# Kernel optimization log

Hardware: AMD Instinct MI355X
Metric: run time of the kernel (lower is better)

## Reference

```python
import jax, jax.numpy as jnp
import numpy as np

NUM_Q_HEADS = 32
NUM_KV_HEADS = 8
GROUP = NUM_Q_HEADS // NUM_KV_HEADS  # 4, matches hardcoded repeat_interleave(repeats=4)
HEAD_DIM = 128
ROPE_BASE = 10000.0


def _rope_cos_sin(seq_len, head_dim, dtype):
    # [S, D/2] angle tables for rotate-half RoPE
    inv_freq = 1.0 / (ROPE_BASE ** (jnp.arange(0, head_dim, 2, dtype=jnp.float32) / head_dim))
    ang = jnp.arange(seq_len, dtype=jnp.float32)[:, None] * inv_freq[None, :]
    return jnp.cos(ang).astype(dtype), jnp.sin(ang).astype(dtype)


def _apply_rope(x, cos, sin):
    # x: [B, S, H, D]; cos/sin: [S, D/2] broadcast over batch & heads
    x1, x2 = jnp.split(x, 2, axis=-1)
    c = cos[None, :, None, :]
    s = sin[None, :, None, :]
    return jnp.concatenate([x1 * c - x2 * s, x2 * c + x1 * s], axis=-1)


def setup_inputs() -> dict:
    key = jax.random.key(0)
    k1, k2, k3 = jax.random.split(key, 3)
    B, S, E = 2, 2048, 4096
    x = jax.random.normal(k1, (B, S, E), dtype=jnp.float32)
    w_in = jax.random.normal(k2, (6144, E), dtype=jnp.float32) * 0.02   # torch Linear weight [out, in]
    w_out = jax.random.normal(k3, (E, E), dtype=jnp.float32) * 0.02
    return {"x": x, "w_in": w_in, "w_out": w_out}


def reference(x, w_in, w_out):
    B, S, E = x.shape
    D = HEAD_DIM
    qkv = jnp.einsum('bse,fe->bsf', x, w_in)  # [B, S, 6144]
    parts = jnp.split(qkv, GROUP + 2, axis=-1)  # 6 equal chunks of width E//GROUP
    q = jnp.concatenate(parts[:GROUP], axis=-1).reshape(B, S, NUM_Q_HEADS, D)
    k = parts[GROUP].reshape(B, S, NUM_KV_HEADS, D)
    v = parts[GROUP + 1].reshape(B, S, NUM_KV_HEADS, D)

    cos, sin = _rope_cos_sin(S, D, x.dtype)
    q = _apply_rope(q, cos, sin)
    k = _apply_rope(k, cos, sin)

    # GQA without materializing repeated K/V: group q heads by kv head.
    # repeat_interleave(k, 4, dim=2) maps q head h -> kv head h // 4, i.e. q view [B,S,HKV,G,D]
    qg = q.reshape(B, S, NUM_KV_HEADS, GROUP, D)
    scale = 1.0 / jnp.sqrt(jnp.asarray(D, dtype=x.dtype))
    scores = jnp.einsum('bqhgd,bkhd->bhgqk', qg, k) * scale  # [B, HKV, G, S, S]
    causal = jnp.tril(jnp.ones((S, S), dtype=bool))
    scores = jnp.where(causal[None, None, None, :, :], scores, jnp.asarray(-1e30, dtype=scores.dtype))
    probs = jax.nn.softmax(scores, axis=-1)
    out = jnp.einsum('bhgqk,bkhd->bqhgd', probs, v)  # [B, S, HKV, G, D]
    out = out.reshape(B, S, E)
    return jnp.einsum('bse,fe->bsf', out, w_out)
```

## Files before the change

### kernel.cpp

```cpp
#include <hip/hip_runtime.h>
#include <hip/hip_bf16.h>
#include <stdint.h>

typedef unsigned short u16;
typedef __bf16 bf16x8 __attribute__((ext_vector_type(8)));
typedef u16 u16x8 __attribute__((ext_vector_type(8)));
typedef float f32x4 __attribute__((ext_vector_type(4)));
typedef float f32x16 __attribute__((ext_vector_type(16)));
typedef uint32_t u32x4 __attribute__((ext_vector_type(4)));

#define DEV __device__ __forceinline__
#define SBAR() asm volatile("s_barrier" ::: "memory")

DEV u16 f2bf(float f) {
  uint32_t u = __builtin_bit_cast(uint32_t, f);
  return (u16)((u + 0x7FFFu + ((u >> 16) & 1u)) >> 16);
}
DEV float bf2f(u16 h) { return __builtin_bit_cast(float, (uint32_t)h << 16); }

DEV void gload_lds16(const void* g, void* l) {
  __builtin_amdgcn_global_load_lds((const __attribute__((address_space(1))) uint32_t*)g,
                                   (__attribute__((address_space(3))) uint32_t*)l, 16, 0, 0);
}

DEV uint32_t cvtpk(float lo, float hi) {
  uint32_t r;
  asm("v_cvt_pk_bf16_f32 %0, %1, %2" : "=v"(r) : "v"(lo), "v"(hi));
  return r;
}
DEV void plswap(uint32_t& a, uint32_t& b) {
  asm("v_permlane32_swap_b32 %0, %1" : "+v"(a), "+v"(b));
}

__global__ void cvt_bf16(const float* __restrict__ in, u16* __restrict__ out, int n) {
  int i = (blockIdx.x * 256 + threadIdx.x) * 8;
  if (i >= n) return;
  const float4* p = reinterpret_cast<const float4*>(in + i);
  float4 a = p[0], b = p[1];
  u16x8 o;
  o[0] = f2bf(a.x); o[1] = f2bf(a.y); o[2] = f2bf(a.z); o[3] = f2bf(a.w);
  o[4] = f2bf(b.x); o[5] = f2bf(b.y); o[6] = f2bf(b.z); o[7] = f2bf(b.w);
  *reinterpret_cast<u16x8*>(out + i) = o;
}

__global__ void rope_table(float* __restrict__ ct, float* __restrict__ st) {
  int i = blockIdx.x * 256 + threadIdx.x;
  int s = i >> 6, d = i & 63;
  float invf = powf(10000.0f, -(float)d * (1.0f / 64.0f));
  float ang = (float)s * invf;
  ct[i] = cosf(ang);
  st[i] = sinf(ang);
}

__global__ void rope_apply(u16* __restrict__ qkv, const float* __restrict__ ct, const float* __restrict__ st) {
  int idx = blockIdx.x * 256 + threadIdx.x;
  int grp = idx & 7;
  int head = (idx >> 3) % 40;
  int row = idx / 320;
  int s = row & 2047;
  size_t f0 = head < 32 ? (size_t)head * 128 : (size_t)4096 + (size_t)(head - 32) * 128;
  u16* p = qkv + (size_t)row * 6144 + f0 + grp * 8;
  u16x8 a = *reinterpret_cast<const u16x8*>(p);
  u16x8 b = *reinterpret_cast<const u16x8*>(p + 64);
  const float4* cp = reinterpret_cast<const float4*>(ct + s * 64 + grp * 8);
  const float4* sp = reinterpret_cast<const float4*>(st + s * 64 + grp * 8);
  float4 c0 = cp[0], c1 = cp[1], s0 = sp[0], s1 = sp[1];
  float cc[8] = {c0.x, c0.y, c0.z, c0.w, c1.x, c1.y, c1.z, c1.w};
  float ss[8] = {s0.x, s0.y, s0.z, s0.w, s1.x, s1.y, s1.z, s1.w};
  u16x8 o1, o2;
#pragma unroll
  for (int i = 0; i < 8; i++) {
    float x1 = bf2f(a[i]), x2 = bf2f(b[i]);
    o1[i] = f2bf(x1 * cc[i] - x2 * ss[i]);
    o2[i] = f2bf(x2 * cc[i] + x1 * ss[i]);
  }
  *reinterpret_cast<u16x8*>(p) = o1;
  *reinterpret_cast<u16x8*>(p + 64) = o2;
}

__global__ void prep_vt(const u16* __restrict__ qkv, u16* __restrict__ vtg) {
  int id = blockIdx.x;
  int j = id & 31, kvh = (id >> 5) & 7, b = id >> 8;
  const int tid = threadIdx.x;
  const size_t rowB = (size_t)b * 2048;
  u16* img = vtg + (size_t)id * 8192;
#pragma unroll
  for (int p = 0; p < 4; p++) {
    int lin = p * 256 + tid;
    int d = lin >> 3, c = lin & 7;
    const u16* src = qkv + (rowB + j * 64 + c * 8) * 6144 + 5120 + kvh * 128 + d;
    u16x8 v;
#pragma unroll
    for (int i = 0; i < 8; i++) v[i] = src[(size_t)i * 6144];
    *reinterpret_cast<u16x8*>(img + d * 64 + ((c ^ (d & 7)) << 3)) = v;
  }
}

DEV void store_c(float* C, size_t idx, float v) { C[idx] = v; }
DEV void store_c(u16* C, size_t idx, float v) { C[idx] = f2bf(v); }

template <typename OutT>
__global__ __launch_bounds__(512, 2) void gemm256(const u16* __restrict__ A, const u16* __restrict__ B,
                                                  OutT* __restrict__ C, int M, int N, int K, int ldc) {
  __shared__ __align__(16) u16 lds[65536];
  char* LB = (char*)lds;
  const int tid = threadIdx.x;
  const int w = tid >> 6, lane = tid & 63;
  const int l15 = lane & 15, l4 = lane >> 4;
  const int wm = w >> 2, wn = w & 3;

  int nwg = gridDim.x;
  int q = nwg >> 3, rr = nwg & 7;
  int xcd = blockIdx.x & 7, idx = blockIdx.x >> 3;
  int sw = (xcd < rr ? xcd * (q + 1) : rr * (q + 1) + (xcd - rr) * q) + idx;
  int gxn = N >> 8;
  int by = sw / gxn, bx = sw - by * gxn;
  const int row0 = by << 8, col0 = bx << 8;
  const int NT = K >> 6;

  const int srow = w * 8 + (lane >> 3);
  const int sc16 = (lane & 7) ^ ((lane >> 3) & 7);
  const u16* gA = A + (size_t)(row0 + srow) * K + sc16 * 8;
  const u16* gB = B + (size_t)(col0 + srow) * K + sc16 * 8;

  const int fl = (l15 & 7) << 4;
  const int aoff = (wm * 128 + l15) * 128 + l4 * 16;
  const int boff = (wn * 64 + l15) * 128 + l4 * 16;

  f32x4 acc[8][4] = {};
  bf16x8 fA[4][2], fB0[2][2], fBc[2][2];

#define STAGE_A(kt, h, base)                                                      \
  {                                                                               \
    const u16* g_ = gA + (size_t)((h)*128) * K + (size_t)(kt)*64;                 \
    gload_lds16(g_, (base) + (h)*16384 + w * 1024);                               \
    gload_lds16(g_ + (size_t)64 * K, (base) + (h)*16384 + 8192 + w * 1024);       \
  }
#define STAGE_B(kt, h, base)                                                      \
  {                                                                               \
    const u16* g_ = gB + (size_t)((h)*128) * K + (size_t)(kt)*64;                 \
    gload_lds16(g_, (base) + (h)*16384 + w * 1024);                               \
    gload_lds16(g_ + (size_t)64 * K, (base) + (h)*16384 + 8192 + w * 1024);       \
  }
#define MFMA_Q(FB, MH, NH)                                                        \
  _Pragma("unroll") for (int kk = 0; kk < 2; kk++) {                              \
    _Pragma("unroll") for (int mf = 0; mf < 4; mf++) {                            \
      _Pragma("unroll") for (int nf = 0; nf < 2; nf++) {                          \
        acc[(MH)*4 + mf][(NH)*2 + nf] = __builtin_amdgcn_mfma_f32_16x16x32_bf16(  \
            fA[mf][kk], FB[nf][kk], acc[(MH)*4 + mf][(NH)*2 + nf], 0, 0, 0);      \
      }                                                                           \
    }                                                                             \
  }

  STAGE_A(0, 0, LB);
  STAGE_A(0, 1, LB);
  STAGE_B(0, 0, LB + 65536);
  STAGE_B(0, 1, LB + 65536);
  STAGE_A(1, 0, LB + 32768);
  STAGE_B(1, 0, LB + 98304);
  STAGE_B(1, 1, LB + 98304);
  asm volatile("s_waitcnt vmcnt(6)" ::: "memory");
  SBAR();

  for (int t = 0; t < NT; ++t) {
    char* ac = LB + (t & 1) * 32768;
    char* bc = LB + 65536 + (t & 1) * 32768;
    char* an = LB + ((t + 1) & 1) * 32768;

#pragma unroll
    for (int mf = 0; mf < 4; mf++)
#pragma unroll
      for (int kk = 0; kk < 2; kk++)
        fA[mf][kk] = *(const bf16x8*)(ac + ((aoff + mf * 2048 + kk * 64) ^ fl));
#pragma unroll
    for (int nf = 0; nf < 2; nf++)
#pragma unroll
      for (int kk = 0; kk < 2; kk++)
        fB0[nf][kk] = *(const bf16x8*)(bc + ((boff + nf * 2048 + kk * 64) ^ fl));
    if (t + 1 < NT) STAGE_A(t + 1, 1, an);
    asm volatile("s_waitcnt lgkmcnt(8)" ::: "memory");
    SBAR();
    asm volatile("s_waitcnt lgkmcnt(0)" ::: "memory");
    __builtin_amdgcn_sched_barrier(0);
    __builtin_amdgcn_s_setprio(1);
    MFMA_Q(fB0, 0, 0);
    __builtin_amdgcn_s_setprio(0);
    SBAR();

#pragma unroll
    for (int nf = 0; nf < 2; nf++)
#pragma unroll
      for (int kk = 0; kk < 2; kk++)
        fBc[nf][kk] = *(const bf16x8*)(bc + ((boff + (nf + 2) * 2048 + kk * 64) ^ fl));
    SBAR();
    asm volatile("s_waitcnt lgkmcnt(0)" ::: "memory");
    __builtin_amdgcn_sched_barrier(0);
    __builtin_amdgcn_s_setprio(1);
    MFMA_Q(fBc, 0, 1);
    __builtin_amdgcn_s_setprio(0);
    SBAR();

#pragma unroll
    for (int mf = 0; mf < 4; mf++)
#pragma unroll
      for (int kk = 0; kk < 2; kk++)
        fA[mf][kk] = *(const bf16x8*)(ac + ((aoff + (mf + 4) * 2048 + kk * 64) ^ fl));
    if (t + 2 < NT) STAGE_B(t + 2, 0, bc);
    SBAR();
    asm volatile("s_waitcnt lgkmcnt(0)" ::: "memory");
    __builtin_amdgcn_sched_barrier(0);
    __builtin_amdgcn_s_setprio(1);
    MFMA_Q(fBc, 1, 1);
    __builtin_amdgcn_s_setprio(0);
    SBAR();

    if (t + 2 < NT) {
      STAGE_A(t + 2, 0, ac);
      STAGE_B(t + 2, 1, bc);
    }
    SBAR();
    __builtin_amdgcn_s_setprio(1);
    MFMA_Q(fB0, 1, 0);
    __builtin_amdgcn_s_setprio(0);
    if (t <= NT - 3) {
      asm volatile("s_waitcnt vmcnt(6)" ::: "memory");
      SBAR();
    } else if (t < NT - 1) {
      asm volatile("s_waitcnt vmcnt(0)" ::: "memory");
      SBAR();
    }
  }

#pragma unroll
  for (int mf = 0; mf < 8; mf++)
#pragma unroll
    for (int nf = 0; nf < 4; nf++)
#pragma unroll
      for (int r = 0; r < 4; r++) {
        size_t row = (size_t)row0 + wm * 128 + mf * 16 + l4 * 4 + r;
        size_t col = (size_t)col0 + wn * 64 + nf * 16 + l15;
        store_c(C, row * (size_t)ldc + col, acc[mf][nf][r]);
      }
#undef STAGE_A
#undef STAGE_B
#undef MFMA_Q
}

__global__ __launch_bounds__(512, 2) void gemm_bn128(const u16* __restrict__ A, const u16* __restrict__ B,
                                                     u16* __restrict__ C, int M, int N, int K, int ldc) {
  __shared__ __align__(16) u16 lds[49152];
  char* LB = (char*)lds;
  const int tid = threadIdx.x;
  const int w = tid >> 6, lane = tid & 63;
  const int l15 = lane & 15, l4 = lane >> 4;
  const int wm = w >> 2, wn = w & 3;

  int nwg = gridDim.x;
  int q = nwg >> 3, rr = nwg & 7;
  int xcd = blockIdx.x & 7, idx = blockIdx.x >> 3;
  int sw = (xcd < rr ? xcd * (q + 1) : rr * (q + 1) + (xcd - rr) * q) + idx;
  int gxn = N >> 7;
  int by = sw / gxn, bx = sw - by * gxn;
  const int row0 = by << 8, col0 = bx << 7;
  const int NT = K >> 6;

  const int srow = w * 8 + (lane >> 3);
  const int sc16 = (lane & 7) ^ ((lane >> 3) & 7);
  const u16* gA = A + (size_t)(row0 + srow) * K + sc16 * 8;
  const u16* gB = B + (size_t)(col0 + srow) * K + sc16 * 8;

  const int fl = (l15 & 7) << 4;
  const int aoff = (wm * 128 + l15) * 128 + l4 * 16;
  const int boff = (wn * 32 + l15) * 128 + l4 * 16;

  f32x4 acc[8][2] = {};
  bf16x8 fA[4][2], fB[2][2];

#define STAGE_A(kt, h, base)                                                      \
  {                                                                               \
    const u16* g_ = gA + (size_t)((h)*128) * K + (size_t)(kt)*64;                 \
    gload_lds16(g_, (base) + (h)*16384 + w * 1024);                               \
    gload_lds16(g_ + (size_t)64 * K, (base) + (h)*16384 + 8192 + w * 1024);       \
  }
#define STAGE_B(kt, base)                                                         \
  {                                                                               \
    const u16* g_ = gB + (size_t)(kt)*64;                                         \
    gload_lds16(g_, (base) + w * 1024);                                           \
    gload_lds16(g_ + (size_t)64 * K, (base) + 8192 + w * 1024);                   \
  }

  STAGE_A(0, 0, LB);
  STAGE_A(0, 1, LB);
  STAGE_B(0, LB + 65536);
  STAGE_A(1, 0, LB + 32768);
  STAGE_B(1, LB + 65536 + 16384);
  asm volatile("s_waitcnt vmcnt(4)" ::: "memory");
  SBAR();

  for (int t = 0; t < NT; ++t) {
    char* ac = LB + (t & 1) * 32768;
    char* bc = LB + 65536 + (t & 1) * 16384;
    char* an = LB + ((t + 1) & 1) * 32768;

#pragma unroll
    for (int mf = 0; mf < 4; mf++)
#pragma unroll
      for (int kk = 0; kk < 2; kk++)
        fA[mf][kk] = *(const bf16x8*)(ac + ((aoff + mf * 2048 + kk * 64) ^ fl));
#pragma unroll
    for (int nf = 0; nf < 2; nf++)
#pragma unroll
      for (int kk = 0; kk < 2; kk++)
        fB[nf][kk] = *(const bf16x8*)(bc + ((boff + nf * 2048 + kk * 64) ^ fl));
    if (t + 1 < NT) STAGE_A(t + 1, 1, an);
    asm volatile("s_waitcnt lgkmcnt(8)" ::: "memory");
    SBAR();
    asm volatile("s_waitcnt lgkmcnt(0)" ::: "memory");
    __builtin_amdgcn_sched_barrier(0);
    __builtin_amdgcn_s_setprio(1);
#pragma unroll
    for (int kk = 0; kk < 2; kk++)
#pragma unroll
      for (int mf = 0; mf < 4; mf++)
#pragma unroll
        for (int nf = 0; nf < 2; nf++)
          acc[mf][nf] = __builtin_amdgcn_mfma_f32_16x16x32_bf16(fA[mf][kk], fB[nf][kk], acc[mf][nf], 0, 0, 0);
    __builtin_amdgcn_s_setprio(0);
    SBAR();

#pragma unroll
    for (int mf = 0; mf < 4; mf++)
#pragma unroll
      for (int kk = 0; kk < 2; kk++)
        fA[mf][kk] = *(const bf16x8*)(ac + ((aoff + (mf + 4) * 2048 + kk * 64) ^ fl));
    if (t + 2 < NT) {
      STAGE_A(t + 2, 0, ac);
      STAGE_B(t + 2, bc);
    }
    SBAR();
    asm volatile("s_waitcnt lgkmcnt(0)" ::: "memory");
    __builtin_amdgcn_sched_barrier(0);
    __builtin_amdgcn_s_setprio(1);
#pragma unroll
    for (int kk = 0; kk < 2; kk++)
#pragma unroll
      for (int mf = 0; mf < 4; mf++)
#pragma unroll
        for (int nf = 0; nf < 2; nf++)
          acc[mf + 4][nf] = __builtin_amdgcn_mfma_f32_16x16x32_bf16(fA[mf][kk], fB[nf][kk], acc[mf + 4][nf], 0, 0, 0);
    __builtin_amdgcn_s_setprio(0);
    if (t <= NT - 3) {
      asm volatile("s_waitcnt vmcnt(4)" ::: "memory");
      SBAR();
    } else if (t < NT - 1) {
      asm volatile("s_waitcnt vmcnt(0)" ::: "memory");
      SBAR();
    }
  }

#pragma unroll
  for (int mf = 0; mf < 8; mf++)
#pragma unroll
    for (int nf = 0; nf < 2; nf++)
#pragma unroll
      for (int r = 0; r < 4; r++) {
        size_t row = (size_t)row0 + wm * 128 + mf * 16 + l4 * 4 + r;
        size_t col = (size_t)col0 + wn * 32 + nf * 16 + l15;
        C[row * (size_t)ldc + col] = f2bf(acc[mf][nf][r]);
      }
#undef STAGE_A
#undef STAGE_B
}

__global__ __launch_bounds__(256, 2) void attn_fwd(const u16* __restrict__ qkv,
                                                   const u16* __restrict__ vtg,
                                                   u16* __restrict__ out) {
  constexpr int S = 2048, F = 6144, E = 4096;
  __shared__ __align__(16) u16 Kt[2 * 8192];
  __shared__ __align__(16) u16 Vt[2 * 8192];

  const int tid = threadIdx.x;
  const int w = tid >> 6, lane = tid & 63;
  const int l31 = lane & 31, hi = lane >> 5;
  const int pair = blockIdx.x;
  const int b = blockIdx.y >> 5, h = blockIdx.y & 31, kvh = h >> 2;
  const size_t rowB = (size_t)b * S;
  const float sc = 0.08838834764831845f * 1.4426950408889634f;
  const int sgn = tid >> 4, sgc = tid & 15;
  const size_t vtb = (size_t)(b * 8 + kvh) * 32 * 8192;

  auto stage = [&](int j, int buf) {
    char* kd = ((char*)Kt) + buf * 16384 + w * 1024;
    char* vd = ((char*)Vt) + buf * 16384 + w * 1024;
    const u16* vs = vtg + vtb + (size_t)j * 8192 + tid * 8;
#pragma unroll
    for (int p = 0; p < 4; p++) {
      int n = p * 16 + sgn;
      const u16* g = qkv + (rowB + j * 64 + n) * F + 4096 + kvh * 128 + (sgc ^ (n & 7)) * 8;
      gload_lds16(g, kd + p * 4096);
      gload_lds16(vs + p * 2048, vd + p * 4096);
    }
  };

  for (int half = 0; half < 2; ++half) {
    const int t = half ? 15 - pair : pair;
    const int nt = 2 * t + 2;
    const int r0 = t * 128;
    const int qg = r0 + w * 32 + l31;

    bf16x8 qf[8];
    {
      const u16* qp = qkv + (rowB + qg) * F + h * 128 + hi * 8;
#pragma unroll
      for (int ds = 0; ds < 8; ds++) qf[ds] = *reinterpret_cast<const bf16x8*>(qp + ds * 16);
    }

    f32x16 acco[4] = {};
    float m = -1e30f, l = 0.f;

    stage(0, 0);
    __syncthreads();

    for (int j = 0; j < nt; ++j) {
      const int cur = j & 1;
      if (j + 1 < nt) stage(j + 1, cur ^ 1);

      const char* kbase = ((const char*)Kt) + cur * 16384;
      f32x16 s0 = {}, s1 = {};
      __builtin_amdgcn_s_setprio(1);
#pragma unroll
      for (int ds = 0; ds < 8; ds++) {
        int ch = ((2 * ds + hi) ^ (l31 & 7)) << 4;
        bf16x8 k0 = *reinterpret_cast<const bf16x8*>(kbase + l31 * 256 + ch);
        bf16x8 k1 = *reinterpret_cast<const bf16x8*>(kbase + (32 + l31) * 256 + ch);
        s0 = __builtin_amdgcn_mfma_f32_32x32x16_bf16(k0, qf[ds], s0, 0, 0, 0);
        s1 = __builtin_amdgcn_mfma_f32_32x32x16_bf16(k1, qf[ds], s1, 0, 0, 0);
      }
      __builtin_amdgcn_s_setprio(0);

      f32x16 px0, px1;
      if (j >= 2 * t) {
#pragma unroll
        for (int rg = 0; rg < 16; rg++) {
          int kv0 = j * 64 + (rg & 3) + 8 * (rg >> 2) + 4 * hi;
          px0[rg] = (kv0 > qg) ? -1e30f : s0[rg] * sc;
          px1[rg] = (kv0 + 32 > qg) ? -1e30f : s1[rg] * sc;
        }
      } else {
#pragma unroll
        for (int rg = 0; rg < 16; rg++) {
          px0[rg] = s0[rg] * sc;
          px1[rg] = s1[rg] * sc;
        }
      }

      float mt[8];
#pragma unroll
      for (int i = 0; i < 8; i++)
        mt[i] = fmaxf(fmaxf(px0[i], px0[i + 8]), fmaxf(px1[i], px1[i + 8]));
#pragma unroll
      for (int stp = 4; stp; stp >>= 1)
#pragma unroll
        for (int i = 0; i < stp; i++) mt[i] = fmaxf(mt[i], mt[i + stp]);
      float pm = fmaxf(mt[0], __shfl_xor(mt[0], 32));

      if (__any(pm > m + 8.0f)) {
        float mn = fmaxf(m, pm);
        float fr = exp2f(m - mn);
        m = mn;
        l *= fr;
#pragma unroll
        for (int rg = 0; rg < 16; rg++) {
          int qrow = (rg & 3) + 8 * (rg >> 2) + 4 * hi;
          float frq = __builtin_bit_cast(
              float, __builtin_amdgcn_ds_bpermute(qrow << 2, __builtin_bit_cast(int, fr)));
          acco[0][rg] *= frq;
          acco[1][rg] *= frq;
          acco[2][rg] *= frq;
          acco[3][rg] *= frq;
        }
      }

#pragma unroll
      for (int rg = 0; rg < 16; rg++) {
        px0[rg] = exp2f(px0[rg] - m);
        px1[rg] = exp2f(px1[rg] - m);
      }
      float at[8];
#pragma unroll
      for (int i = 0; i < 8; i++)
        at[i] = (px0[i] + px0[i + 8]) + (px1[i] + px1[i + 8]);
#pragma unroll
      for (int stp = 4; stp; stp >>= 1)
#pragma unroll
        for (int i = 0; i < stp; i++) at[i] += at[i + stp];
      l += at[0] + __shfl_xor(at[0], 32);

      const char* vbase = ((const char*)Vt) + cur * 16384;
      __builtin_amdgcn_s_setprio(1);
#define PV_STEP(PH, SS)                                                               \
  {                                                                                   \
    uint32_t X0 = cvtpk(PH[((SS)&1) * 8 + 0], PH[((SS)&1) * 8 + 1]);                  \
    uint32_t Y0 = cvtpk(PH[((SS)&1) * 8 + 4], PH[((SS)&1) * 8 + 5]);                  \
    uint32_t X1 = cvtpk(PH[((SS)&1) * 8 + 2], PH[((SS)&1) * 8 + 3]);                  \
    uint32_t Y1 = cvtpk(PH[((SS)&1) * 8 + 6], PH[((SS)&1) * 8 + 7]);                  \
    plswap(X0, Y0);                                                                   \
    plswap(X1, Y1);                                                                   \
    u32x4 pw = {X0, X1, Y0, Y1};                                                      \
    bf16x8 pa = __builtin_bit_cast(bf16x8, pw);                                       \
    _Pragma("unroll") for (int df = 0; df < 4; df++) {                                \
      bf16x8 vf = *reinterpret_cast<const bf16x8*>(                                   \
          vbase + (32 * df + l31) * 128 + (((2 * (SS) + hi) ^ (l31 & 7)) << 4));      \
      acco[df] = __builtin_amdgcn_mfma_f32_32x32x16_bf16(pa, vf, acco[df], 0, 0, 0);  \
    }                                                                                 \
  }
      PV_STEP(px0, 0)
      PV_STEP(px0, 1)
      PV_STEP(px1, 2)
      PV_STEP(px1, 3)
#undef PV_STEP
      __builtin_amdgcn_s_setprio(0);

      __syncthreads();
    }

    float linv = 1.f / l;
#pragma unroll
    for (int rg = 0; rg < 16; rg++) {
      int qrow = (rg & 3) + 8 * (rg >> 2) + 4 * hi;
      float lv = __builtin_bit_cast(
          float, __builtin_amdgcn_ds_bpermute(qrow << 2, __builtin_bit_cast(int, linv)));
      size_t row = rowB + r0 + w * 32 + qrow;
      u16* op = out + row * E + h * 128 + l31;
#pragma unroll
      for (int df = 0; df < 4; df++) op[df * 32] = f2bf(acco[df][rg] * lv);
    }
  }
}

extern "C" void kernel_launch(void* const* d_in, const int* in_sizes, int n_in,
                              void* d_out, int out_size, void* d_ws, size_t ws_size,
                              hipStream_t stream) {
  const float* x = (const float*)d_in[0];
  const float* w_in = (const float*)d_in[1];
  const float* w_out = (const float*)d_in[2];
  float* out = (float*)d_out;
  char* ws = (char*)d_ws;

  u16* xb = (u16*)(ws);
  u16* wib = (u16*)(ws + 33554432ull);
  u16* wob = (u16*)(ws + 83886080ull);
  u16* qkvb = (u16*)(ws + 117440512ull);
  float* ct = (float*)(ws + 167772160ull);
  float* st = ct + 2048 * 64;
  u16* attnb = xb;
  u16* vtg = wib;

  cvt_bf16<<<8192, 256, 0, stream>>>(x, xb, 16777216);
  cvt_bf16<<<12288, 256, 0, stream>>>(w_in, wib, 25165824);
  cvt_bf16<<<8192, 256, 0, stream>>>(w_out, wob, 16777216);
  rope_table<<<512, 256, 0, stream>>>(ct, st);
  gemm256<u16><<<256, 512, 0, stream>>>(xb, wib, qkvb, 4096, 4096, 4096, 6144);
  gemm_bn128<<<256, 512, 0, stream>>>(xb, wib + (size_t)4096 * 4096, qkvb + 4096, 4096, 2048, 4096, 6144);
  rope_apply<<<5120, 256, 0, stream>>>(qkvb, ct, st);
  prep_vt<<<512, 256, 0, stream>>>(qkvb, vtg);
  attn_fwd<<<dim3(8, 64), 256, 0, stream>>>(qkvb, vtg, attnb);
  gemm256<float><<<256, 512, 0, stream>>>(attnb, wob, out, 4096, 4096, 4096, 4096);
}
```

Measured before the change: 511.1 us.

## Cut per-iteration barriers in GEMM main loops and issue LDS reads ahead of MFMAs

Restructures the inner-loop schedule of both bf16 GEMM kernels. The next-tile A stage is issued first, all B fragment reads are hoisted before the first MFMA group, and the global-to-LDS restaging for tile t+2 is grouped after a single mid-iteration barrier. This removes several s_barrier calls per iteration and uses partial lgkmcnt waits. Fewer barriers can let waves drift apart and overlap LDS reads with MFMAs, at the risk of LDS buffer hazards if the remaining barriers do not cover every reuse.

```diff
diff --git a/kernel.cpp b/kernel.cpp
--- a/kernel.cpp
+++ b/kernel.cpp
@@ -11,6 +11,7 @@
 
 #define DEV __device__ __forceinline__
 #define SBAR() asm volatile("s_barrier" ::: "memory")
+#define SCHEDB() __builtin_amdgcn_sched_barrier(0)
 
 DEV u16 f2bf(float f) {
   uint32_t u = __builtin_bit_cast(uint32_t, f);
@@ -167,65 +168,62 @@
     char* bc = LB + 65536 + (t & 1) * 32768;
     char* an = LB + ((t + 1) & 1) * 32768;
 
+    if (t + 1 < NT) STAGE_A(t + 1, 1, an);
+
 #pragma unroll
     for (int mf = 0; mf < 4; mf++)
 #pragma unroll
       for (int kk = 0; kk < 2; kk++)
         fA[mf][kk] = *(const bf16x8*)(ac + ((aoff + mf * 2048 + kk * 64) ^ fl));
+    SCHEDB();
 #pragma unroll
     for (int nf = 0; nf < 2; nf++)
 #pragma unroll
       for (int kk = 0; kk < 2; kk++)
         fB0[nf][kk] = *(const bf16x8*)(bc + ((boff + nf * 2048 + kk * 64) ^ fl));
-    if (t + 1 < NT) STAGE_A(t + 1, 1, an);
-    asm volatile("s_waitcnt lgkmcnt(8)" ::: "memory");
-    SBAR();
-    asm volatile("s_waitcnt lgkmcnt(0)" ::: "memory");
-    __builtin_amdgcn_sched_barrier(0);
+    SCHEDB();
+#pragma unroll
+    for (int nf = 0; nf < 2; nf++)
+#pragma unroll
+      for (int kk = 0; kk < 2; kk++)
+        fBc[nf][kk] = *(const bf16x8*)(bc + ((boff + (nf + 2) * 2048 + kk * 64) ^ fl));
+    SCHEDB();
+
+    asm volatile("s_waitcnt lgkmcnt(4)" ::: "memory");
+    SCHEDB();
     __builtin_amdgcn_s_setprio(1);
     MFMA_Q(fB0, 0, 0);
     __builtin_amdgcn_s_setprio(0);
-    SBAR();
-
-#pragma unroll
-    for (int nf = 0; nf < 2; nf++)
-#pragma unroll
-      for (int kk = 0; kk < 2; kk++)
-        fBc[nf][kk] = *(const bf16x8*)(bc + ((boff + (nf + 2) * 2048 + kk * 64) ^ fl));
-    SBAR();
+
     asm volatile("s_waitcnt lgkmcnt(0)" ::: "memory");
-    __builtin_amdgcn_sched_barrier(0);
+    SCHEDB();
     __builtin_amdgcn_s_setprio(1);
     MFMA_Q(fBc, 0, 1);
     __builtin_amdgcn_s_setprio(0);
+
+#pragma unroll
+    for (int mf = 0; mf < 4; mf++)
+#pragma unroll
+      for (int kk = 0; kk < 2; kk++)
+        fA[mf][kk] = *(const bf16x8*)(ac + ((aoff + (mf + 4) * 2048 + kk * 64) ^ fl));
+    asm volatile("s_waitcnt lgkmcnt(0)" ::: "memory");
+    SCHEDB();
+
     SBAR();
-
-#pragma unroll
-    for (int mf = 0; mf < 4; mf++)
-#pragma unroll
-      for (int kk = 0; kk < 2; kk++)
-        fA[mf][kk] = *(const bf16x8*)(ac + ((aoff + (mf + 4) * 2048 + kk * 64) ^ fl));
-    if (t + 2 < NT) STAGE_B(t + 2, 0, bc);
-    SBAR();
-    asm volatile("s_waitcnt lgkmcnt(0)" ::: "memory");
-    __builtin_amdgcn_sched_barrier(0);
+    if (t + 2 < NT) {
+      STAGE_B(t + 2, 0, bc);
+      STAGE_B(t + 2, 1, bc);
+      STAGE_A(t + 2, 0, ac);
+    }
     __builtin_amdgcn_s_setprio(1);
     MFMA_Q(fBc, 1, 1);
-    __builtin_amdgcn_s_setprio(0);
-    SBAR();
-
-    if (t + 2 < NT) {
-      STAGE_A(t + 2, 0, ac);
-      STAGE_B(t + 2, 1, bc);
-    }
-    SBAR();
-    __builtin_amdgcn_s_setprio(1);
     MFMA_Q(fB0, 1, 0);
     __builtin_amdgcn_s_setprio(0);
-    if (t <= NT - 3) {
+
+    if (t + 2 < NT) {
       asm volatile("s_waitcnt vmcnt(6)" ::: "memory");
       SBAR();
-    } else if (t < NT - 1) {
+    } else if (t + 1 < NT) {
       asm volatile("s_waitcnt vmcnt(0)" ::: "memory");
       SBAR();
     }
@@ -302,6 +300,8 @@
     char* bc = LB + 65536 + (t & 1) * 16384;
     char* an = LB + ((t + 1) & 1) * 32768;
 
+    if (t + 1 < NT) STAGE_A(t + 1, 1, an);
+
 #pragma unroll
     for (int mf = 0; mf < 4; mf++)
 #pragma unroll
@@ -312,11 +312,9 @@
 #pragma unroll
       for (int kk = 0; kk < 2; kk++)
         fB[nf][kk] = *(const bf16x8*)(bc + ((boff + nf * 2048 + kk * 64) ^ fl));
-    if (t + 1 < NT) STAGE_A(t + 1, 1, an);
-    asm volatile("s_waitcnt lgkmcnt(8)" ::: "memory");
-    SBAR();
+    SCHEDB();
     asm volatile("s_waitcnt lgkmcnt(0)" ::: "memory");
-    __builtin_amdgcn_sched_barrier(0);
+    SCHEDB();
     __builtin_amdgcn_s_setprio(1);
 #pragma unroll
     for (int kk = 0; kk < 2; kk++)
@@ -326,20 +324,20 @@
         for (int nf = 0; nf < 2; nf++)
           acc[mf][nf] = __builtin_amdgcn_mfma_f32_16x16x32_bf16(fA[mf][kk], fB[nf][kk], acc[mf][nf], 0, 0, 0);
     __builtin_amdgcn_s_setprio(0);
+
+#pragma unroll
+    for (int mf = 0; mf < 4; mf++)
+#pragma unroll
+      for (int kk = 0; kk < 2; kk++)
+        fA[mf][kk] = *(const bf16x8*)(ac + ((aoff + (mf + 4) * 2048 + kk * 64) ^ fl));
+    asm volatile("s_waitcnt lgkmcnt(0)" ::: "memory");
+    SCHEDB();
+
     SBAR();
-
-#pragma unroll
-    for (int mf = 0; mf < 4; mf++)
-#pragma unroll
-      for (int kk = 0; kk < 2; kk++)
-        fA[mf][kk] = *(const bf16x8*)(ac + ((aoff + (mf + 4) * 2048 + kk * 64) ^ fl));
     if (t + 2 < NT) {
       STAGE_A(t + 2, 0, ac);
       STAGE_B(t + 2, bc);
     }
-    SBAR();
-    asm volatile("s_waitcnt lgkmcnt(0)" ::: "memory");
-    __builtin_amdgcn_sched_barrier(0);
     __builtin_amdgcn_s_setprio(1);
 #pragma unroll
     for (int kk = 0; kk < 2; kk++)
@@ -349,10 +347,11 @@
         for (int nf = 0; nf < 2; nf++)
           acc[mf + 4][nf] = __builtin_amdgcn_mfma_f32_16x16x32_bf16(fA[mf][kk], fB[nf][kk], acc[mf + 4][nf], 0, 0, 0);
     __builtin_amdgcn_s_setprio(0);
-    if (t <= NT - 3) {
+
+    if (t + 2 < NT) {
       asm volatile("s_waitcnt vmcnt(4)" ::: "memory");
       SBAR();
-    } else if (t < NT - 1) {
+    } else if (t + 1 < NT) {
       asm volatile("s_waitcnt vmcnt(0)" ::: "memory");
       SBAR();
     }
```

Result: no change. 507.6 us (-0.7%).
